# Optimization experiments

Hardware: AMD Instinct MI355X
Metric: run time of the kernel (lower is better)

Reference implementation:

```python
import jax, jax.numpy as jnp
import numpy as np

N_HEADS = 16
HEAD_DIM = 128  # dim // n_heads = 2048 // 16

def setup_inputs() -> dict:
    key = jax.random.key(0)
    ks = jax.random.split(key, 7)
    B, S, D = 2, 2048, 2048
    scale = 0.02
    return {
        "q": jax.random.normal(ks[0], (B, S, D), dtype=jnp.float32),
        "k": jax.random.normal(ks[1], (B, S, D), dtype=jnp.float32),
        "v": jax.random.normal(ks[2], (B, S, D), dtype=jnp.float32),
        "wq": jax.random.normal(ks[3], (D, D), dtype=jnp.float32) * scale,
        "wk": jax.random.normal(ks[4], (D, D), dtype=jnp.float32) * scale,
        "wv": jax.random.normal(ks[5], (D, D), dtype=jnp.float32) * scale,
        "wo": jax.random.normal(ks[6], (D, D), dtype=jnp.float32) * scale,
    }

def reference(q, k, v, wq, wk, wv, wo):
    B, S, _ = q.shape
    # Linear (no bias): torch Linear computes x @ W.T; weights here stored as [out, in]
    xq = (q @ wq.T).reshape(B, S, N_HEADS, HEAD_DIM).transpose(0, 2, 1, 3)  # [B,H,S,d]
    xk = (k @ wk.T).reshape(B, S, N_HEADS, HEAD_DIM).transpose(0, 2, 1, 3)
    xv = (v @ wv.T).reshape(B, S, N_HEADS, HEAD_DIM).transpose(0, 2, 1, 3)
    scores = jnp.einsum("bhqd,bhkd->bhqk", xq, xk) / jnp.sqrt(jnp.float32(HEAD_DIM))
    # causal mask: -inf above the diagonal
    causal = jnp.tril(jnp.ones((S, S), dtype=bool))
    scores = jnp.where(causal[None, None], scores, -jnp.inf)
    attn = jax.nn.softmax(scores.astype(jnp.float32), axis=-1)  # dropout is identity at eval
    out = jnp.einsum("bhqk,bhkd->bhqd", attn, xv)
    out = out.transpose(0, 2, 1, 3).reshape(B, S, N_HEADS * HEAD_DIM)
    return out @ wo.T
```

## Files before the change

### kernel.cpp

```cpp
#include <hip/hip_runtime.h>
#include <hip/hip_bf16.h>

#define B_ 2
#define S_ 2048
#define D_ 2048
#define H_ 16
#define HD_ 128

typedef __attribute__((ext_vector_type(4))) float f32x4;
typedef __attribute__((ext_vector_type(8))) short bf16x8;

static __device__ __forceinline__ unsigned short f2bf(float f) {
    unsigned int u = __float_as_uint(f);
    u += 0x7fffu + ((u >> 16) & 1u);
    return (unsigned short)(u >> 16);
}
static __device__ __forceinline__ float bf2f(unsigned short h) {
    return __uint_as_float(((unsigned int)h) << 16);
}

#define MFMA_K32(a, b, c) __builtin_amdgcn_mfma_f32_16x16x32_bf16(a, b, c, 0, 0, 0)

static __device__ __forceinline__ void gll16(const void* g, void* l) {
    __builtin_amdgcn_global_load_lds((const __attribute__((address_space(1))) void*)g,
                                     (__attribute__((address_space(3))) void*)l,
                                     16, 0, 0);
}

__global__ void cvt_in(const float4* __restrict__ src, ushort4* __restrict__ dst) {
    int i = blockIdx.x * 256 + threadIdx.x;
    float4 v = src[i];
    ushort4 o;
    o.x = f2bf(v.x); o.y = f2bf(v.y); o.z = f2bf(v.z); o.w = f2bf(v.w);
    dst[i] = o;
}

__global__ void cvt_w4(const float4* __restrict__ s0, ushort4* __restrict__ d0,
                       const float4* __restrict__ s1, ushort4* __restrict__ d1,
                       const float4* __restrict__ s2, ushort4* __restrict__ d2,
                       const float4* __restrict__ s3, ushort4* __restrict__ d3) {
    const float4* s; ushort4* d;
    switch (blockIdx.y) {
        case 0: s = s0; d = d0; break;
        case 1: s = s1; d = d1; break;
        case 2: s = s2; d = d2; break;
        default: s = s3; d = d3; break;
    }
    int i = blockIdx.x * 256 + threadIdx.x;
    float4 v = s[i];
    ushort4 o;
    o.x = f2bf(v.x); o.y = f2bf(v.y); o.z = f2bf(v.z); o.w = f2bf(v.w);
    d[i] = o;
}

template<int OUT_MODE>
__global__ __launch_bounds__(256) void gemm_xwt(
        const unsigned short* __restrict__ A,
        const unsigned short* __restrict__ W,
        void* __restrict__ C) {
    constexpr int K = D_;
    __shared__ unsigned short As[128 * 32];
    __shared__ unsigned short Ws[128 * 32];
    const int tid = threadIdx.x, lane = tid & 63, wid = tid >> 6;
    const int wy = wid >> 1, wx = wid & 1;
    const int g = lane >> 4, lr = lane & 15;
    const int swz = (blockIdx.x & 7) * 64 + (blockIdx.x >> 3);
    const int bm = (swz & 31) * 128;
    const int bn = (swz >> 5) * 128;

    const int ch0 = wid * 128 + lane;
    const int r0 = ch0 >> 2, c0 = (ch0 & 3) * 8;
    const int ch1 = ch0 + 64;
    const int r1 = ch1 >> 2, c1 = (ch1 & 3) * 8;

    f32x4 acc[4][4] = {};
    for (int k0 = 0; k0 < K; k0 += 32) {
        __syncthreads();
        gll16(A + (size_t)(bm + r0) * K + k0 + c0, (char*)As + wid * 2048);
        gll16(A + (size_t)(bm + r1) * K + k0 + c1, (char*)As + wid * 2048 + 1024);
        gll16(W + (size_t)(bn + r0) * K + k0 + c0, (char*)Ws + wid * 2048);
        gll16(W + (size_t)(bn + r1) * K + k0 + c1, (char*)Ws + wid * 2048 + 1024);
        __syncthreads();
        bf16x8 af[4], wf[4];
        #pragma unroll
        for (int i = 0; i < 4; ++i)
            af[i] = *(const bf16x8*)((const char*)As + (wy * 64 + i * 16 + lr) * 64 + g * 16);
        #pragma unroll
        for (int i = 0; i < 4; ++i)
            wf[i] = *(const bf16x8*)((const char*)Ws + (wx * 64 + i * 16 + lr) * 64 + g * 16);
        #pragma unroll
        for (int mi = 0; mi < 4; ++mi)
            #pragma unroll
            for (int ni = 0; ni < 4; ++ni)
                acc[mi][ni] = MFMA_K32(af[mi], wf[ni], acc[mi][ni]);
    }

    #pragma unroll
    for (int mi = 0; mi < 4; ++mi) {
        #pragma unroll
        for (int ni = 0; ni < 4; ++ni) {
            const int n = bn + wx * 64 + ni * 16 + lr;
            const int m0 = bm + wy * 64 + mi * 16 + g * 4;
            if constexpr (OUT_MODE == 0) {
                #pragma unroll
                for (int rg = 0; rg < 4; ++rg) {
                    int m = m0 + rg;
                    int bb = m >> 11, s = m & (S_ - 1);
                    int hh = n >> 7, dd = n & (HD_ - 1);
                    ((unsigned short*)C)[(((size_t)(bb * H_ + hh) * S_) + s) * HD_ + dd] =
                        f2bf(acc[mi][ni][rg]);
                }
            } else if constexpr (OUT_MODE == 1) {
                #pragma unroll
                for (int rg = 0; rg < 4; ++rg) {
                    int m = m0 + rg;
                    int bb = m >> 11, s = m & (S_ - 1);
                    int hh = n >> 7, dd = n & (HD_ - 1);
                    int vr = s & 63;
                    int pr = (vr & 3) | (((vr >> 3) & 3) << 2) | (((vr >> 2) & 1) << 4) | (vr & 32);
                    size_t eo = ((size_t)(bb * H_ + hh) << 18) + ((size_t)(s >> 6) << 13)
                              + pr * 128 + (((((unsigned)dd) << 1) ^ ((pr & 7) << 4)) >> 1);
                    ((unsigned short*)C)[eo] = f2bf(acc[mi][ni][rg]);
                }
            } else if constexpr (OUT_MODE == 2) {
                int bb = m0 >> 11, s0 = m0 & (S_ - 1);
                int hh = n >> 7, dd = n & (HD_ - 1);
                int ch = ((s0 & 63) >> 3) ^ (dd & 7);
                size_t eo = ((size_t)(bb * H_ + hh) << 18) + ((size_t)(s0 >> 6) << 13)
                          + dd * 64 + (ch << 3) + (s0 & 7);
                ushort4 pk;
                pk.x = f2bf(acc[mi][ni][0]); pk.y = f2bf(acc[mi][ni][1]);
                pk.z = f2bf(acc[mi][ni][2]); pk.w = f2bf(acc[mi][ni][3]);
                *(ushort4*)&((unsigned short*)C)[eo] = pk;
            } else {
                #pragma unroll
                for (int rg = 0; rg < 4; ++rg)
                    ((float*)C)[(size_t)(m0 + rg) * D_ + n] = acc[mi][ni][rg];
            }
        }
    }
}

__global__ __launch_bounds__(256) void attn_fwd(
        const unsigned short* __restrict__ Qg,
        const unsigned short* __restrict__ Kt,
        const unsigned short* __restrict__ Vt,
        unsigned short* __restrict__ Og) {
    __shared__ char Ks[16384];
    __shared__ char Vs[16384];
    const int tid = threadIdx.x, lane = tid & 63, w = tid >> 6;
    const int g = lane >> 4, lr = lane & 15;
    const int swz = (blockIdx.x & 7) * 64 + (blockIdx.x >> 3);
    const int bh = swz >> 4, qi = swz & 15;
    const int b = bh >> 4, h = bh & (H_ - 1);
    const size_t base = (size_t)bh * S_ * HD_;

    #pragma unroll 1
    for (int half = 0; half < 2; ++half) {
        const int q0 = (half ? (31 - qi) : qi) * 64;
        const int qr = q0 + w * 16 + lr;
        bf16x8 qf[4];
        #pragma unroll
        for (int st = 0; st < 4; ++st) {
            bf16x8 t = *(const bf16x8*)(Qg + base + (size_t)qr * HD_ + st * 32 + g * 8);
            #pragma unroll
            for (int j = 0; j < 8; ++j)
                t[j] = (short)f2bf(bf2f((unsigned short)t[j]) * 0.08838834764831845f);
            qf[st] = t;
        }
        float m_r = -1e30f, l_r = 0.0f;
        f32x4 accO[8] = {};
        const int nt = (q0 >> 6) + 1;
        for (int t = 0; t < nt; ++t) {
            __syncthreads();
            const size_t tb = base + (size_t)t * 8192 + w * 2048 + lane * 8;
            gll16(Kt + tb,        Ks + w * 4096);
            gll16(Kt + tb + 512,  Ks + w * 4096 + 1024);
            gll16(Kt + tb + 1024, Ks + w * 4096 + 2048);
            gll16(Kt + tb + 1536, Ks + w * 4096 + 3072);
            gll16(Vt + tb,        Vs + w * 4096);
            gll16(Vt + tb + 512,  Vs + w * 4096 + 1024);
            gll16(Vt + tb + 1024, Vs + w * 4096 + 2048);
            gll16(Vt + tb + 1536, Vs + w * 4096 + 3072);
            __syncthreads();

            f32x4 sf[4] = {};
            #pragma unroll
            for (int f = 0; f < 4; ++f) {
                const int row = f * 16 + lr;
                const int sw = (row & 7) << 4;
                #pragma unroll
                for (int st = 0; st < 4; ++st) {
                    bf16x8 kf = *(const bf16x8*)(Ks + row * 256 + ((st * 64 + g * 16) ^ sw));
                    sf[f] = MFMA_K32(kf, qf[st], sf[f]);
                }
            }
            if (t == nt - 1) {
                const int k0 = t * 64;
                #pragma unroll
                for (int f = 0; f < 4; ++f)
                    #pragma unroll
                    for (int rg = 0; rg < 4; ++rg)
                        if (k0 + 32 * (f >> 1) + 8 * g + 4 * (f & 1) + rg > qr)
                            sf[f][rg] = -1e30f;
            }

            float pm = -1e30f;
            #pragma unroll
            for (int f = 0; f < 4; ++f)
                #pragma unroll
                for (int rg = 0; rg < 4; ++rg) pm = fmaxf(pm, sf[f][rg]);
            pm = fmaxf(pm, __shfl_xor(pm, 16));
            pm = fmaxf(pm, __shfl_xor(pm, 32));
            const float mnew = fmaxf(m_r, pm);
            const float corr = __expf(m_r - mnew);
            m_r = mnew;
            float ls = 0.0f;
            bf16x8 plo, phi;
            #pragma unroll
            for (int f = 0; f < 2; ++f)
                #pragma unroll
                for (int rg = 0; rg < 4; ++rg) {
                    float p = __expf(sf[f][rg] - mnew);
                    ls += p;
                    plo[f * 4 + rg] = (short)f2bf(p);
                }
            #pragma unroll
            for (int f = 0; f < 2; ++f)
                #pragma unroll
                for (int rg = 0; rg < 4; ++rg) {
                    float p = __expf(sf[2 + f][rg] - mnew);
                    ls += p;
                    phi[f * 4 + rg] = (short)f2bf(p);
                }
            ls += __shfl_xor(ls, 16);
            ls += __shfl_xor(ls, 32);
            l_r = l_r * corr + ls;

            float cj[4];
            #pragma unroll
            for (int j = 0; j < 4; ++j) cj[j] = __shfl(corr, g * 4 + j);
            #pragma unroll
            for (int db = 0; db < 8; ++db) {
                accO[db][0] *= cj[0]; accO[db][1] *= cj[1];
                accO[db][2] *= cj[2]; accO[db][3] *= cj[3];
            }

            #pragma unroll
            for (int db = 0; db < 8; ++db) {
                const int d = db * 16 + lr;
                bf16x8 vlo = *(const bf16x8*)(Vs + d * 128 + ((g ^ (d & 7)) << 4));
                accO[db] = MFMA_K32(plo, vlo, accO[db]);
            }
            #pragma unroll
            for (int db = 0; db < 8; ++db) {
                const int d = db * 16 + lr;
                bf16x8 vhi = *(const bf16x8*)(Vs + d * 128 + (((4 + g) ^ (d & 7)) << 4));
                accO[db] = MFMA_K32(phi, vhi, accO[db]);
            }
        }

        float lj[4];
        #pragma unroll
        for (int j = 0; j < 4; ++j) lj[j] = __shfl(l_r, g * 4 + j);
        #pragma unroll
        for (int j = 0; j < 4; ++j) {
            const int qq = q0 + w * 16 + g * 4 + j;
            const float inv = 1.0f / lj[j];
            unsigned short* dst = Og + ((size_t)(b * S_ + qq)) * D_ + h * HD_;
            #pragma unroll
            for (int db = 0; db < 8; ++db)
                dst[db * 16 + lr] = f2bf(accO[db][j] * inv);
        }
    }
}

extern "C" void kernel_launch(void* const* d_in, const int* in_sizes, int n_in,
                              void* d_out, int out_size, void* d_ws, size_t ws_size,
                              hipStream_t stream) {
    const float* q  = (const float*)d_in[0];
    const float* k  = (const float*)d_in[1];
    const float* v  = (const float*)d_in[2];
    const float* wq = (const float*)d_in[3];
    const float* wk = (const float*)d_in[4];
    const float* wv = (const float*)d_in[5];
    const float* wo = (const float*)d_in[6];

    unsigned short* ws   = (unsigned short*)d_ws;
    unsigned short* wqb  = ws;
    unsigned short* wkb  = wqb + (size_t)D_ * D_;
    unsigned short* wvb  = wkb + (size_t)D_ * D_;
    unsigned short* wob  = wvb + (size_t)D_ * D_;
    unsigned short* xq   = wob + (size_t)D_ * D_;
    unsigned short* xk   = xq + (size_t)B_ * S_ * D_;
    unsigned short* xv   = xk + (size_t)B_ * S_ * D_;
    unsigned short* slot = xv + (size_t)B_ * S_ * D_;

    cvt_w4<<<dim3(4096, 4), 256, 0, stream>>>(
        (const float4*)wq, (ushort4*)wqb, (const float4*)wk, (ushort4*)wkb,
        (const float4*)wv, (ushort4*)wvb, (const float4*)wo, (ushort4*)wob);

    cvt_in<<<8192, 256, 0, stream>>>((const float4*)q, (ushort4*)slot);
    gemm_xwt<0><<<512, 256, 0, stream>>>(slot, wqb, xq);
    cvt_in<<<8192, 256, 0, stream>>>((const float4*)k, (ushort4*)slot);
    gemm_xwt<1><<<512, 256, 0, stream>>>(slot, wkb, xk);
    cvt_in<<<8192, 256, 0, stream>>>((const float4*)v, (ushort4*)slot);
    gemm_xwt<2><<<512, 256, 0, stream>>>(slot, wvb, xv);

    attn_fwd<<<512, 256, 0, stream>>>(xq, xk, xv, slot);

    gemm_xwt<3><<<512, 256, 0, stream>>>(slot, wob, d_out);
}
```

Before: 327.8 us.

## Fuse input conversion into GEMMs, double-buffer tiles, widen attention query tiles

The GEMM now loads fp32 activations directly, converts them to bf16 in registers and writes them to a double-buffered LDS tile, which removes the three separate cvt_in passes. Both the GEMM and the attention kernel prefetch the next K/V or A/W tile into a second LDS buffer while computing on the current one. Attention processes 128 query rows per block as two 64-row sub-tiles that share each K/V tile, halving the grid, and switches to exp2 with the log2e factor folded into the Q scale, plus s_setprio around MFMA regions. The cost is doubled LDS and more registers, which may reduce occupancy, and only half as many attention blocks.

```diff
diff --git a/kernel.cpp b/kernel.cpp
--- a/kernel.cpp
+++ b/kernel.cpp
@@ -18,6 +18,14 @@
 static __device__ __forceinline__ float bf2f(unsigned short h) {
     return __uint_as_float(((unsigned int)h) << 16);
 }
+static __device__ __forceinline__ bf16x8 pack8(float4 a, float4 b) {
+    bf16x8 o;
+    o[0] = (short)f2bf(a.x); o[1] = (short)f2bf(a.y);
+    o[2] = (short)f2bf(a.z); o[3] = (short)f2bf(a.w);
+    o[4] = (short)f2bf(b.x); o[5] = (short)f2bf(b.y);
+    o[6] = (short)f2bf(b.z); o[7] = (short)f2bf(b.w);
+    return o;
+}
 
 #define MFMA_K32(a, b, c) __builtin_amdgcn_mfma_f32_16x16x32_bf16(a, b, c, 0, 0, 0)
 
@@ -25,14 +33,6 @@
     __builtin_amdgcn_global_load_lds((const __attribute__((address_space(1))) void*)g,
                                      (__attribute__((address_space(3))) void*)l,
                                      16, 0, 0);
-}
-
-__global__ void cvt_in(const float4* __restrict__ src, ushort4* __restrict__ dst) {
-    int i = blockIdx.x * 256 + threadIdx.x;
-    float4 v = src[i];
-    ushort4 o;
-    o.x = f2bf(v.x); o.y = f2bf(v.y); o.z = f2bf(v.z); o.w = f2bf(v.w);
-    dst[i] = o;
 }
 
 __global__ void cvt_w4(const float4* __restrict__ s0, ushort4* __restrict__ d0,
@@ -53,14 +53,14 @@
     d[i] = o;
 }
 
-template<int OUT_MODE>
+template<int OUT_MODE, bool A_F32>
 __global__ __launch_bounds__(256) void gemm_xwt(
-        const unsigned short* __restrict__ A,
+        const void* __restrict__ Aptr,
         const unsigned short* __restrict__ W,
         void* __restrict__ C) {
     constexpr int K = D_;
-    __shared__ unsigned short As[128 * 32];
-    __shared__ unsigned short Ws[128 * 32];
+    __shared__ unsigned short As[2][128 * 32];
+    __shared__ unsigned short Ws[2][128 * 32];
     const int tid = threadIdx.x, lane = tid & 63, wid = tid >> 6;
     const int wy = wid >> 1, wx = wid & 1;
     const int g = lane >> 4, lr = lane & 15;
@@ -68,31 +68,60 @@
     const int bm = (swz & 31) * 128;
     const int bn = (swz >> 5) * 128;
 
-    const int ch0 = wid * 128 + lane;
-    const int r0 = ch0 >> 2, c0 = (ch0 & 3) * 8;
-    const int ch1 = ch0 + 64;
-    const int r1 = ch1 >> 2, c1 = (ch1 & 3) * 8;
+    const int r0 = (wid * 128 + lane) >> 2, c0 = (lane & 3) * 8;
+    const int r1 = r0 + 16;
+    const int ar = tid >> 2, ac = (tid & 3) * 8;
+
+    const float* Af = (const float*)Aptr;
+    const unsigned short* Ab = (const unsigned short*)Aptr;
 
     f32x4 acc[4][4] = {};
+    float4 Ar0, Ar1, Ar2, Ar3;
+
+    auto stageW = [&](int k0, int nb) {
+        gll16(W + (size_t)(bn + r0) * K + k0 + c0, (char*)&Ws[nb][0] + wid * 2048);
+        gll16(W + (size_t)(bn + r1) * K + k0 + c0, (char*)&Ws[nb][0] + wid * 2048 + 1024);
+    };
+    auto stageAb = [&](int k0, int nb) {
+        gll16(Ab + (size_t)(bm + r0) * K + k0 + c0, (char*)&As[nb][0] + wid * 2048);
+        gll16(Ab + (size_t)(bm + r1) * K + k0 + c0, (char*)&As[nb][0] + wid * 2048 + 1024);
+    };
+    auto loadA = [&](int k0) {
+        const float* p = Af + (size_t)(bm + ar) * K + k0 + ac;
+        Ar0 = *(const float4*)p; Ar1 = *(const float4*)(p + 4);
+        const float* p2 = Af + (size_t)(bm + 64 + ar) * K + k0 + ac;
+        Ar2 = *(const float4*)p2; Ar3 = *(const float4*)(p2 + 4);
+    };
+    auto writeA = [&](int nb) {
+        *(bf16x8*)&As[nb][ar * 32 + ac] = pack8(Ar0, Ar1);
+        *(bf16x8*)&As[nb][(64 + ar) * 32 + ac] = pack8(Ar2, Ar3);
+    };
+
+    stageW(0, 0);
+    if constexpr (A_F32) { loadA(0); writeA(0); } else { stageAb(0, 0); }
+    int cur = 0;
+
     for (int k0 = 0; k0 < K; k0 += 32) {
         __syncthreads();
-        gll16(A + (size_t)(bm + r0) * K + k0 + c0, (char*)As + wid * 2048);
-        gll16(A + (size_t)(bm + r1) * K + k0 + c1, (char*)As + wid * 2048 + 1024);
-        gll16(W + (size_t)(bn + r0) * K + k0 + c0, (char*)Ws + wid * 2048);
-        gll16(W + (size_t)(bn + r1) * K + k0 + c1, (char*)Ws + wid * 2048 + 1024);
-        __syncthreads();
+        const bool nxt = (k0 + 32 < K);
+        if (nxt) {
+            stageW(k0 + 32, cur ^ 1);
+            if constexpr (A_F32) loadA(k0 + 32); else stageAb(k0 + 32, cur ^ 1);
+        }
         bf16x8 af[4], wf[4];
         #pragma unroll
         for (int i = 0; i < 4; ++i)
-            af[i] = *(const bf16x8*)((const char*)As + (wy * 64 + i * 16 + lr) * 64 + g * 16);
+            af[i] = *(const bf16x8*)((const char*)&As[cur][0] + (wy * 64 + i * 16 + lr) * 64 + g * 16);
         #pragma unroll
         for (int i = 0; i < 4; ++i)
-            wf[i] = *(const bf16x8*)((const char*)Ws + (wx * 64 + i * 16 + lr) * 64 + g * 16);
+            wf[i] = *(const bf16x8*)((const char*)&Ws[cur][0] + (wx * 64 + i * 16 + lr) * 64 + g * 16);
         #pragma unroll
         for (int mi = 0; mi < 4; ++mi)
             #pragma unroll
             for (int ni = 0; ni < 4; ++ni)
                 acc[mi][ni] = MFMA_K32(af[mi], wf[ni], acc[mi][ni]);
+        if (nxt) { if constexpr (A_F32) writeA(cur ^ 1); }
+        cur ^= 1;
     }
 
     #pragma unroll
@@ -146,131 +175,177 @@
         const unsigned short* __restrict__ Kt,
         const unsigned short* __restrict__ Vt,
         unsigned short* __restrict__ Og) {
-    __shared__ char Ks[16384];
-    __shared__ char Vs[16384];
+    __shared__ char Ks[2][16384];
+    __shared__ char Vs[2][16384];
     const int tid = threadIdx.x, lane = tid & 63, w = tid >> 6;
     const int g = lane >> 4, lr = lane & 15;
-    const int swz = (blockIdx.x & 7) * 64 + (blockIdx.x >> 3);
-    const int bh = swz >> 4, qi = swz & 15;
+    const int swz = (blockIdx.x & 7) * 32 + (blockIdx.x >> 3);
+    const int bh = swz >> 3, pi = swz & 7;
     const int b = bh >> 4, h = bh & (H_ - 1);
     const size_t base = (size_t)bh * S_ * HD_;
-
+    const float SCL = 0.08838834764831845f * 1.4426950408889634f;
+
+    auto stage = [&](int t, int nb) {
+        const size_t tb = base + (size_t)t * 8192 + w * 2048 + (size_t)lane * 8;
+        char* kd = &Ks[nb][0] + w * 4096;
+        char* vd = &Vs[nb][0] + w * 4096;
+        gll16(Kt + tb, kd);        gll16(Kt + tb + 512, kd + 1024);
+        gll16(Kt + tb + 1024, kd + 2048); gll16(Kt + tb + 1536, kd + 3072);
+        gll16(Vt + tb, vd);        gll16(Vt + tb + 512, vd + 1024);
+        gll16(Vt + tb + 1024, vd + 2048); gll16(Vt + tb + 1536, vd + 3072);
+    };
+
+    int cur = 0;
     #pragma unroll 1
     for (int half = 0; half < 2; ++half) {
-        const int q0 = (half ? (31 - qi) : qi) * 64;
-        const int qr = q0 + w * 16 + lr;
-        bf16x8 qf[4];
+        const int qt = half ? (15 - pi) : pi;
+        const int q0 = qt * 128;
+        const int qrA = q0 + w * 16 + lr, qrB = qrA + 64;
+
+        bf16x8 qfA[4], qfB[4];
         #pragma unroll
         for (int st = 0; st < 4; ++st) {
-            bf16x8 t = *(const bf16x8*)(Qg + base + (size_t)qr * HD_ + st * 32 + g * 8);
-            #pragma unroll
-            for (int j = 0; j < 8; ++j)
-                t[j] = (short)f2bf(bf2f((unsigned short)t[j]) * 0.08838834764831845f);
-            qf[st] = t;
-        }
-        float m_r = -1e30f, l_r = 0.0f;
-        f32x4 accO[8] = {};
-        const int nt = (q0 >> 6) + 1;
+            bf16x8 ta = *(const bf16x8*)(Qg + base + (size_t)qrA * HD_ + st * 32 + g * 8);
+            bf16x8 tb2 = *(const bf16x8*)(Qg + base + (size_t)qrB * HD_ + st * 32 + g * 8);
+            #pragma unroll
+            for (int j = 0; j < 8; ++j) {
+                ta[j] = (short)f2bf(bf2f((unsigned short)ta[j]) * SCL);
+                tb2[j] = (short)f2bf(bf2f((unsigned short)tb2[j]) * SCL);
+            }
+            qfA[st] = ta; qfB[st] = tb2;
+        }
+
+        float mA = -1e30f, lA = 0.0f, mB = -1e30f, lB = 0.0f;
+        f32x4 accA[8] = {}, accB[8] = {};
+        const int nt = qt * 2 + 2;
+
+        stage(0, cur);
+
         for (int t = 0; t < nt; ++t) {
             __syncthreads();
-            const size_t tb = base + (size_t)t * 8192 + w * 2048 + lane * 8;
-            gll16(Kt + tb,        Ks + w * 4096);
-            gll16(Kt + tb + 512,  Ks + w * 4096 + 1024);
-            gll16(Kt + tb + 1024, Ks + w * 4096 + 2048);
-            gll16(Kt + tb + 1536, Ks + w * 4096 + 3072);
-            gll16(Vt + tb,        Vs + w * 4096);
-            gll16(Vt + tb + 512,  Vs + w * 4096 + 1024);
-            gll16(Vt + tb + 1024, Vs + w * 4096 + 2048);
-            gll16(Vt + tb + 1536, Vs + w * 4096 + 3072);
-            __syncthreads();
-
-            f32x4 sf[4] = {};
+            if (t + 1 < nt) stage(t + 1, cur ^ 1);
+            const char* Kb = &Ks[cur][0];
+            const char* Vb = &Vs[cur][0];
+            const bool actA = (t < nt - 1);
+
+            f32x4 sA[4] = {}, sB[4] = {};
+            __builtin_amdgcn_s_setprio(1);
             #pragma unroll
             for (int f = 0; f < 4; ++f) {
                 const int row = f * 16 + lr;
                 const int sw = (row & 7) << 4;
                 #pragma unroll
                 for (int st = 0; st < 4; ++st) {
-                    bf16x8 kf = *(const bf16x8*)(Ks + row * 256 + ((st * 64 + g * 16) ^ sw));
-                    sf[f] = MFMA_K32(kf, qf[st], sf[f]);
-                }
+                    bf16x8 kf = *(const bf16x8*)(Kb + row * 256 + ((st * 64 + g * 16) ^ sw));
+                    if (actA) sA[f] = MFMA_K32(kf, qfA[st], sA[f]);
+                    sB[f] = MFMA_K32(kf, qfB[st], sB[f]);
+                }
+            }
+            __builtin_amdgcn_s_setprio(0);
+
+            if (t == nt - 2) {
+                #pragma unroll
+                for (int f = 0; f < 4; ++f)
+                    #pragma unroll
+                    for (int rg = 0; rg < 4; ++rg)
+                        if (q0 + 32 * (f >> 1) + 8 * g + 4 * (f & 1) + rg > qrA)
+                            sA[f][rg] = -1e30f;
             }
             if (t == nt - 1) {
-                const int k0 = t * 64;
                 #pragma unroll
                 for (int f = 0; f < 4; ++f)
                     #pragma unroll
                     for (int rg = 0; rg < 4; ++rg)
-                        if (k0 + 32 * (f >> 1) + 8 * g + 4 * (f & 1) + rg > qr)
-                            sf[f][rg] = -1e30f;
-            }
-
-            float pm = -1e30f;
-            #pragma unroll
-            for (int f = 0; f < 4; ++f)
-                #pragma unroll
-                for (int rg = 0; rg < 4; ++rg) pm = fmaxf(pm, sf[f][rg]);
-            pm = fmaxf(pm, __shfl_xor(pm, 16));
-            pm = fmaxf(pm, __shfl_xor(pm, 32));
-            const float mnew = fmaxf(m_r, pm);
-            const float corr = __expf(m_r - mnew);
-            m_r = mnew;
-            float ls = 0.0f;
-            bf16x8 plo, phi;
-            #pragma unroll
-            for (int f = 0; f < 2; ++f)
-                #pragma unroll
-                for (int rg = 0; rg < 4; ++rg) {
-                    float p = __expf(sf[f][rg] - mnew);
-                    ls += p;
-                    plo[f * 4 + rg] = (short)f2bf(p);
-                }
-            #pragma unroll
-            for (int f = 0; f < 2; ++f)
-                #pragma unroll
-                for (int rg = 0; rg < 4; ++rg) {
-                    float p = __expf(sf[2 + f][rg] - mnew);
-                    ls += p;
-                    phi[f * 4 + rg] = (short)f2bf(p);
-                }
-            ls += __shfl_xor(ls, 16);
-            ls += __shfl_xor(ls, 32);
-            l_r = l_r * corr + ls;
-
-            float cj[4];
-            #pragma unroll
-            for (int j = 0; j < 4; ++j) cj[j] = __shfl(corr, g * 4 + j);
-            #pragma unroll
-            for (int db = 0; db < 8; ++db) {
-                accO[db][0] *= cj[0]; accO[db][1] *= cj[1];
-                accO[db][2] *= cj[2]; accO[db][3] *= cj[3];
-            }
-
+                        if (q0 + 64 + 32 * (f >> 1) + 8 * g + 4 * (f & 1) + rg > qrB)
+                            sB[f][rg] = -1e30f;
+            }
+
+            bf16x8 pAlo, pAhi, pBlo, pBhi;
+            auto softmax_step = [&](f32x4* sf, float& m_r, float& l_r, f32x4* accO,
+                                    bf16x8& plo, bf16x8& phi) {
+                float pm = -1e30f;
+                #pragma unroll
+                for (int f = 0; f < 4; ++f)
+                    #pragma unroll
+                    for (int rg = 0; rg < 4; ++rg) pm = fmaxf(pm, sf[f][rg]);
+                pm = fmaxf(pm, __shfl_xor(pm, 16));
+                pm = fmaxf(pm, __shfl_xor(pm, 32));
+                const float mnew = fmaxf(m_r, pm);
+                const float corr = exp2f(m_r - mnew);
+                m_r = mnew;
+                float ls = 0.0f;
+                #pragma unroll
+                for (int f = 0; f < 2; ++f)
+                    #pragma unroll
+                    for (int rg = 0; rg < 4; ++rg) {
+                        float p = exp2f(sf[f][rg] - mnew);
+                        ls += p;
+                        plo[f * 4 + rg] = (short)f2bf(p);
+                    }
+                #pragma unroll
+                for (int f = 0; f < 2; ++f)
+                    #pragma unroll
+                    for (int rg = 0; rg < 4; ++rg) {
+                        float p = exp2f(sf[2 + f][rg] - mnew);
+                        ls += p;
+                        phi[f * 4 + rg] = (short)f2bf(p);
+                    }
+                ls += __shfl_xor(ls, 16);
+                ls += __shfl_xor(ls, 32);
+                l_r = l_r * corr + ls;
+                float cj[4];
+                #pragma unroll
+                for (int j = 0; j < 4; ++j) cj[j] = __shfl(corr, g * 4 + j);
+                #pragma unroll
+                for (int db = 0; db < 8; ++db) {
+                    accO[db][0] *= cj[0]; accO[db][1] *= cj[1];
+                    accO[db][2] *= cj[2]; accO[db][3] *= cj[3];
+                }
+            };
+            if (actA) softmax_step(sA, mA, lA, accA, pAlo, pAhi);
+            softmax_step(sB, mB, lB, accB, pBlo, pBhi);
+
+            __builtin_amdgcn_s_setprio(1);
             #pragma unroll
             for (int db = 0; db < 8; ++db) {
                 const int d = db * 16 + lr;
-                bf16x8 vlo = *(const bf16x8*)(Vs + d * 128 + ((g ^ (d & 7)) << 4));
-                accO[db] = MFMA_K32(plo, vlo, accO[db]);
-            }
-            #pragma unroll
-            for (int db = 0; db < 8; ++db) {
-                const int d = db * 16 + lr;
-                bf16x8 vhi = *(const bf16x8*)(Vs + d * 128 + (((4 + g) ^ (d & 7)) << 4));
-                accO[db] = MFMA_K32(phi, vhi, accO[db]);
-            }
-        }
-
-        float lj[4];
-        #pragma unroll
-        for (int j = 0; j < 4; ++j) lj[j] = __shfl(l_r, g * 4 + j);
-        #pragma unroll
-        for (int j = 0; j < 4; ++j) {
-            const int qq = q0 + w * 16 + g * 4 + j;
-            const float inv = 1.0f / lj[j];
-            unsigned short* dst = Og + ((size_t)(b * S_ + qq)) * D_ + h * HD_;
-            #pragma unroll
-            for (int db = 0; db < 8; ++db)
-                dst[db * 16 + lr] = f2bf(accO[db][j] * inv);
+                bf16x8 vlo = *(const bf16x8*)(Vb + d * 128 + ((g ^ (d & 7)) << 4));
+                bf16x8 vhi = *(const bf16x8*)(Vb + d * 128 + (((4 + g) ^ (d & 7)) << 4));
+                if (actA) {
+                    accA[db] = MFMA_K32(pAlo, vlo, accA[db]);
+                    accA[db] = MFMA_K32(pAhi, vhi, accA[db]);
+                }
+                accB[db] = MFMA_K32(pBlo, vlo, accB[db]);
+                accB[db] = MFMA_K32(pBhi, vhi, accB[db]);
+            }
+            __builtin_amdgcn_s_setprio(0);
+            cur ^= 1;
+        }
+
+        {
+            float lj[4];
+            #pragma unroll
+            for (int j = 0; j < 4; ++j) lj[j] = __shfl(lA, g * 4 + j);
+            #pragma unroll
+            for (int j = 0; j < 4; ++j) {
+                const int qq = q0 + w * 16 + g * 4 + j;
+                const float inv = 1.0f / lj[j];
+                unsigned short* dst = Og + ((size_t)(b * S_ + qq)) * D_ + h * HD_;
+                #pragma unroll
+                for (int db = 0; db < 8; ++db)
+                    dst[db * 16 + lr] = f2bf(accA[db][j] * inv);
+            }
+            #pragma unroll
+            for (int j = 0; j < 4; ++j) lj[j] = __shfl(lB, g * 4 + j);
+            #pragma unroll
+            for (int j = 0; j < 4; ++j) {
+                const int qq = q0 + 64 + w * 16 + g * 4 + j;
+                const float inv = 1.0f / lj[j];
+                unsigned short* dst = Og + ((size_t)(b * S_ + qq)) * D_ + h * HD_;
+                #pragma unroll
+                for (int db = 0; db < 8; ++db)
+                    dst[db * 16 + lr] = f2bf(accB[db][j] * inv);
+            }
         }
     }
 }
@@ -300,14 +375,11 @@
         (const float4*)wq, (ushort4*)wqb, (const float4*)wk, (ushort4*)wkb,
         (const float4*)wv, (ushort4*)wvb, (const float4*)wo, (ushort4*)wob);
 
-    cvt_in<<<8192, 256, 0, stream>>>((const float4*)q, (ushort4*)slot);
-    gemm_xwt<0><<<512, 256, 0, stream>>>(slot, wqb, xq);
-    cvt_in<<<8192, 256, 0, stream>>>((const float4*)k, (ushort4*)slot);
-    gemm_xwt<1><<<512, 256, 0, stream>>>(slot, wkb, xk);
-    cvt_in<<<8192, 256, 0, stream>>>((const float4*)v, (ushort4*)slot);
-    gemm_xwt<2><<<512, 256, 0, stream>>>(slot, wvb, xv);
-
-    attn_fwd<<<512, 256, 0, stream>>>(xq, xk, xv, slot);
-
-    gemm_xwt<3><<<512, 256, 0, stream>>>(slot, wob, d_out);
-}
+    gemm_xwt<0, true><<<512, 256, 0, stream>>>(q, wqb, xq);
+    gemm_xwt<1, true><<<512, 256, 0, stream>>>(k, wkb, xk);
+    gemm_xwt<2, true><<<512, 256, 0, stream>>>(v, wvb, xv);
+
+    attn_fwd<<<256, 256, 0, stream>>>(xq, xk, xv, slot);
+
+    gemm_xwt<3, false><<<512, 256, 0, stream>>>(slot, wob, d_out);
+}
```

After: 399.0 us. 1.22x slower.
